# Optimization experiments

Measured on AMD Instinct MI355X. Metric: run time of the kernel, lower is better.

The kernel has to match this reference:

```python
import jax, jax.numpy as jnp
from jax import lax
import numpy as np

D_MODEL = 512
N_HEAD = 8
FACTOR = 5
PRED_LEN = 5
LABEL_LEN = 5
B = 8
SRC_LEN = 2048


def make_pe(max_len, d):
    pos = np.arange(max_len, dtype=np.float32)[:, None]
    div = np.exp(np.arange(0, d, 2, dtype=np.float32) * (-np.log(10000.0) / d))
    pe = np.zeros((max_len, d), dtype=np.float32)
    pe[:, 0::2] = np.sin(pos * div)
    pe[:, 1::2] = np.cos(pos * div)
    return jnp.asarray(pe)


def layer_norm(x, g, b):
    mu = x.mean(-1, keepdims=True)
    var = ((x - mu) ** 2).mean(-1, keepdims=True)
    return (x - mu) / jnp.sqrt(var + 1e-5) * g + b


def prob_attention(q, k, v, key):
    # ProbSparse attention, mask_flag=False (Informer encoder). q,k,v: [B,H,L,E]
    Bq, H, L, E = q.shape
    L_K = k.shape[2]
    U_part = min(FACTOR * int(np.ceil(np.log(L_K))), L_K)
    u = min(FACTOR * int(np.ceil(np.log(L))), L)
    idx = jax.random.randint(key, (L, U_part), 0, L_K)  # sampled key ids per query
    k_samp = k[:, :, idx, :]                             # [B,H,L,U,E]
    qk_samp = jnp.einsum('bhle,bhlue->bhlu', q, k_samp)
    M = qk_samp.max(-1) - qk_samp.sum(-1) / L_K          # sparsity measure [B,H,L]
    _, top_idx = lax.top_k(M, u)                         # [B,H,u]
    q_red = jnp.take_along_axis(q, top_idx[..., None], axis=2)       # [B,H,u,E]
    scores = jnp.einsum('bhue,bhle->bhul', q_red, k) / jnp.sqrt(jnp.asarray(E, q.dtype))
    attn = jax.nn.softmax(scores, axis=-1)
    upd = jnp.einsum('bhul,bhle->bhue', attn, v)
    ctx = jnp.broadcast_to(v.mean(axis=2, keepdims=True), (Bq, H, L, E))
    bi = jnp.arange(Bq)[:, None, None]
    hi = jnp.arange(H)[None, :, None]
    ctx = ctx.at[bi, hi, top_idx].set(upd)               # scatter active queries
    return ctx.transpose(0, 2, 1, 3)                     # [B,L,H,E]


def attn_block(x, wq, bq, wk, bk, wv, bv, wo, bo, key):
    Bx, L, D = x.shape
    E = D // N_HEAD
    q = (x @ wq + bq).reshape(Bx, L, N_HEAD, E).transpose(0, 2, 1, 3)
    k = (x @ wk + bk).reshape(Bx, L, N_HEAD, E).transpose(0, 2, 1, 3)
    v = (x @ wv + bv).reshape(Bx, L, N_HEAD, E).transpose(0, 2, 1, 3)
    ctx = prob_attention(q, k, v, key)
    return ctx.reshape(Bx, L, D) @ wo + bo


def distill(x, w, b, g, beta, rm, rv):
    # circular conv k=3 -> BatchNorm(eval) -> ELU -> maxpool k=3 s=2 p=1
    xc = x.transpose(0, 2, 1)
    xp = jnp.pad(xc, ((0, 0), (0, 0), (1, 1)), mode='wrap')
    y = lax.conv_general_dilated(xp, w, (1,), 'VALID',
                                 dimension_numbers=('NCH', 'OIH', 'NCH')) + b[None, :, None]
    y = (y - rm[None, :, None]) / jnp.sqrt(rv[None, :, None] + 1e-5) * g[None, :, None] + beta[None, :, None]
    y = jax.nn.elu(y)
    y = lax.reduce_window(y, -jnp.inf, lax.max, (1, 1, 3), (1, 1, 2),
                          [(0, 0), (0, 0), (1, 1)])
    return y.transpose(0, 2, 1)


def reference(src, tgt_start, in_w, in_b, conv_w, conv_b,
              wq, bq, wk, bk, wv, bv, wo, bo,
              n1_g, n1_b, ff1_w, ff1_b, ff2_w, ff2_b, n2_g, n2_b,
              dconv_w, dconv_b, bn_g, bn_b, bn_m, bn_v,
              enc_g, enc_b, dec_w, dec_b, head_w, head_b):
    Bx, L, _ = src.shape
    pe = make_pe(5000, D_MODEL)
    x = src @ in_w + in_b + pe[:L][None]
    xc = lax.conv_general_dilated(x.transpose(0, 2, 1), conv_w, (1,), [(1, 1)],
                                  dimension_numbers=('NCH', 'OIH', 'NCH')) + conv_b[None, :, None]
    x = xc.transpose(0, 2, 1)
    base = jax.random.key(42)
    n_layers = wq.shape[0]
    for i in range(n_layers):
        key = jax.random.fold_in(base, i)
        a = attn_block(x, wq[i], bq[i], wk[i], bk[i], wv[i], bv[i], wo[i], bo[i], key)
        x = layer_norm(x + a, n1_g[i], n1_b[i])
        y = jax.nn.gelu(x @ ff1_w[i] + ff1_b[i], approximate=False)
        y = y @ ff2_w[i] + ff2_b[i]
        x = layer_norm(x + y, n2_g[i], n2_b[i])
        if i < n_layers - 1:
            x = distill(x, dconv_w[i], dconv_b[i], bn_g[i], bn_b[i], bn_m[i], bn_v[i])
    memory = layer_norm(x, enc_g, enc_b)
    # decoder side of the source forward (self.decoder is never called there)
    dec_len = LABEL_LEN + PRED_LEN
    y0 = jnp.zeros((Bx, dec_len, 2), src.dtype).at[:, :LABEL_LEN, :].set(tgt_start[:, 0, :][:, None, :])
    pe2 = make_pe(2048, D_MODEL)
    tgt = y0 @ dec_w + dec_b + pe2[:dec_len][None]
    # faithful bug: pos_decoder(tgt, memory) treats batch axis as seq axis
    dec_out = tgt + pe2[:Bx][:, None, :]
    out = dec_out @ head_w + head_b
    pred = out[:, -PRED_LEN:, :]
    return pred, memory


def setup_inputs():
    key = jax.random.key(0)
    ks = iter(jax.random.split(key, 64))

    def w(shape, scale):
        return jax.random.normal(next(ks), shape, jnp.float32) * scale

    L4, L3, D = 4, 3, D_MODEL
    s = 1.0 / np.sqrt(D)
    return dict(
        src=jax.random.normal(next(ks), (B, SRC_LEN, 6), jnp.float32),
        tgt_start=jax.random.normal(next(ks), (B, 1, 2), jnp.float32),
        in_w=w((6, D), 1.0 / np.sqrt(6)), in_b=w((D,), 0.02),
        conv_w=w((D, D, 3), 1.0 / np.sqrt(3 * D)), conv_b=w((D,), 0.02),
        wq=w((L4, D, D), s), bq=w((L4, D), 0.02),
        wk=w((L4, D, D), s), bk=w((L4, D), 0.02),
        wv=w((L4, D, D), s), bv=w((L4, D), 0.02),
        wo=w((L4, D, D), s), bo=w((L4, D), 0.02),
        n1_g=jnp.ones((L4, D)), n1_b=jnp.zeros((L4, D)),
        ff1_w=w((L4, D, D), s), ff1_b=w((L4, D), 0.02),
        ff2_w=w((L4, D, D), s), ff2_b=w((L4, D), 0.02),
        n2_g=jnp.ones((L4, D)), n2_b=jnp.zeros((L4, D)),
        dconv_w=w((L3, D, D, 3), 1.0 / np.sqrt(3 * D)), dconv_b=w((L3, D), 0.02),
        bn_g=jnp.ones((L3, D)), bn_b=jnp.zeros((L3, D)),
        bn_m=jnp.zeros((L3, D)), bn_v=jnp.ones((L3, D)),
        enc_g=jnp.ones((D,)), enc_b=jnp.zeros((D,)),
        dec_w=w((2, D), 1.0 / np.sqrt(2)), dec_b=w((D,), 0.02),
        head_w=w((D, 2), s), head_b=w((2,), 0.02),
    )
```

## Files before the change

kernel.cpp:

```cpp
#include <hip/hip_runtime.h>
#include <hip/hip_bf16.h>
#include <math.h>
#include <stdint.h>

typedef long long ll;

__host__ __device__ inline uint32_t rotl32(uint32_t v, int d) { return (v << d) | (v >> (32 - d)); }

#define TF_R4(a, b, c, d)                              \
  x0 += x1; x1 = rotl32(x1, a); x1 ^= x0;              \
  x0 += x1; x1 = rotl32(x1, b); x1 ^= x0;              \
  x0 += x1; x1 = rotl32(x1, c); x1 ^= x0;              \
  x0 += x1; x1 = rotl32(x1, d); x1 ^= x0;

__host__ __device__ inline void threefry(uint32_t k0, uint32_t k1, uint32_t x0, uint32_t x1,
                                         uint32_t* o0, uint32_t* o1) {
  uint32_t ks2 = k0 ^ k1 ^ 0x1BD11BDAu;
  x0 += k0; x1 += k1;
  TF_R4(13, 15, 26, 6)
  x0 += k1; x1 += ks2 + 1u;
  TF_R4(17, 29, 16, 24)
  x0 += ks2; x1 += k0 + 2u;
  TF_R4(13, 15, 26, 6)
  x0 += k0; x1 += k1 + 3u;
  TF_R4(17, 29, 16, 24)
  x0 += k1; x1 += ks2 + 4u;
  TF_R4(13, 15, 26, 6)
  x0 += ks2; x1 += k0 + 5u;
  *o0 = x0; *o1 = x1;
}

__device__ __forceinline__ float pe_val(int pos, int d) {
  int k2 = (d >> 1) << 1;
  float div = expf((float)k2 * (-9.210340371976184f / 512.0f));
  float arg = (float)pos * div;
  return (d & 1) ? cosf(arg) : sinf(arg);
}


__global__ __launch_bounds__(256) void embed_kernel(const float* __restrict__ src,
                                                    const float* __restrict__ in_w,
                                                    const float* __restrict__ in_b,
                                                    int b0, int nb, float* __restrict__ out) {
  ll i = (ll)blockIdx.x * 256 + threadIdx.x;
  if (i >= (ll)nb * 2048 * 512) return;
  int d = (int)(i & 511);
  ll r = i >> 9;
  int l = (int)(r & 2047);
  int b = b0 + (int)(r >> 11);
  float acc = in_b[d];
#pragma unroll
  for (int j = 0; j < 6; j++)
    acc = fmaf(src[((ll)b * 2048 + l) * 6 + j], in_w[j * 512 + d], acc);
  acc += pe_val(l, d);
  out[i] = acc;
}

__global__ __launch_bounds__(256) void wt_kernel(const float* __restrict__ W,
                                                 float* __restrict__ WT,
                                                 ll srcOff) {
  __shared__ float tile[64][65];
  int o0 = blockIdx.x * 64, c0 = blockIdx.y * 64;
  int t = threadIdx.x;
  int g = t >> 6, l = t & 63;
#pragma unroll 4
  for (int jj = 0; jj < 16; jj++) {
    int r = g * 16 + jj;
    tile[r][l] = W[srcOff + (ll)(o0 + r) * 1536 + (c0 + l)];
  }
  __syncthreads();
#pragma unroll 4
  for (int jj = 0; jj < 16; jj++) {
    int c = g * 16 + jj;
    int gc = c0 + c;
    int tap = gc % 3, k = gc / 3;
    WT[(ll)tap * 262144 + (ll)k * 512 + (o0 + l)] = tile[l][c];
  }
}

__global__ __launch_bounds__(256, 4) void gemm_kernel(
    const float* __restrict__ A, int mBase, int L, int K,
    const float* __restrict__ W, ll wOffBase, int wSK, int wSN, int wTapStride,
    const float* __restrict__ bias, float* __restrict__ C, int N,
    int taps, int shiftMode, int fuse,
    const float* __restrict__ bn_g, const float* __restrict__ bn_b,
    const float* __restrict__ bn_m, const float* __restrict__ bn_v) {
  __shared__ float As[32][68];
  __shared__ float Bs[32][64];
  const int tid = threadIdx.x;
  const int tx = tid & 15, ty = tid >> 4;
  const int m0 = blockIdx.x * 64, n0 = blockIdx.y * 64;
  const int rA = tid >> 2;
  const int kA = (tid & 3) << 3;
  const int kB = tid >> 4, nB0 = (tid & 15) << 2;

  float acc[4][4] = {};

  for (int tp = 0; tp < taps; tp++) {
    int shift = (taps == 3) ? tp - 1 : 0;
    int gRow = mBase + m0 + rA;
    int b = gRow / L, l = gRow - b * L;
    int l2 = l + shift;
    bool valid = true;
    if (shiftMode == 1) { valid = (l2 >= 0 && l2 < L); if (!valid) l2 = 0; }
    else if (shiftMode == 2) { l2 = l2 < 0 ? l2 + L : (l2 >= L ? l2 - L : l2); }
    const float* aRow = A + (ll)(b * L + l2) * K;
    const ll wOff = wOffBase + (taps == 3 ? (ll)tp * wTapStride : 0);

    for (int k0 = 0; k0 < K; k0 += 32) {
      float4 a0 = make_float4(0.f, 0.f, 0.f, 0.f);
      float4 a1 = make_float4(0.f, 0.f, 0.f, 0.f);
      if (valid) {
        a0 = *(const float4*)(aRow + k0 + kA);
        a1 = *(const float4*)(aRow + k0 + kA + 4);
      }
      As[kA + 0][rA] = a0.x; As[kA + 1][rA] = a0.y;
      As[kA + 2][rA] = a0.z; As[kA + 3][rA] = a0.w;
      As[kA + 4][rA] = a1.x; As[kA + 5][rA] = a1.y;
      As[kA + 6][rA] = a1.z; As[kA + 7][rA] = a1.w;
      if (wSN == 1) {
        *(float4*)&Bs[kB][nB0] = *(const float4*)(W + wOff + (ll)(k0 + kB) * wSK + (n0 + nB0));
        *(float4*)&Bs[kB + 16][nB0] = *(const float4*)(W + wOff + (ll)(k0 + kB + 16) * wSK + (n0 + nB0));
      } else {
#pragma unroll
        for (int j = 0; j < 4; j++)
          Bs[kB][nB0 + j] = W[wOff + (ll)(k0 + kB) * wSK + (ll)(n0 + nB0 + j) * wSN];
#pragma unroll
        for (int j = 0; j < 4; j++)
          Bs[kB + 16][nB0 + j] = W[wOff + (ll)(k0 + kB + 16) * wSK + (ll)(n0 + nB0 + j) * wSN];
      }
      __syncthreads();
#pragma unroll
      for (int kk = 0; kk < 32; kk++) {
        float4 w4 = *(const float4*)&Bs[kk][tx << 2];
        float4 a4 = *(const float4*)&As[kk][ty << 2];
        acc[0][0] = fmaf(a4.x, w4.x, acc[0][0]); acc[0][1] = fmaf(a4.x, w4.y, acc[0][1]);
        acc[0][2] = fmaf(a4.x, w4.z, acc[0][2]); acc[0][3] = fmaf(a4.x, w4.w, acc[0][3]);
        acc[1][0] = fmaf(a4.y, w4.x, acc[1][0]); acc[1][1] = fmaf(a4.y, w4.y, acc[1][1]);
        acc[1][2] = fmaf(a4.y, w4.z, acc[1][2]); acc[1][3] = fmaf(a4.y, w4.w, acc[1][3]);
        acc[2][0] = fmaf(a4.z, w4.x, acc[2][0]); acc[2][1] = fmaf(a4.z, w4.y, acc[2][1]);
        acc[2][2] = fmaf(a4.z, w4.z, acc[2][2]); acc[2][3] = fmaf(a4.z, w4.w, acc[2][3]);
        acc[3][0] = fmaf(a4.w, w4.x, acc[3][0]); acc[3][1] = fmaf(a4.w, w4.y, acc[3][1]);
        acc[3][2] = fmaf(a4.w, w4.z, acc[3][2]); acc[3][3] = fmaf(a4.w, w4.w, acc[3][3]);
      }
      __syncthreads();
    }
  }

  float4 bv = make_float4(0.f, 0.f, 0.f, 0.f);
  if (bias) bv = *(const float4*)(bias + n0 + (tx << 2));
  float4 g4, b4, m4, v4;
  if (fuse == 2) {
    g4 = *(const float4*)(bn_g + n0 + (tx << 2));
    b4 = *(const float4*)(bn_b + n0 + (tx << 2));
    m4 = *(const float4*)(bn_m + n0 + (tx << 2));
    v4 = *(const float4*)(bn_v + n0 + (tx << 2));
    v4.x = 1.f / sqrtf(v4.x + 1e-5f); v4.y = 1.f / sqrtf(v4.y + 1e-5f);
    v4.z = 1.f / sqrtf(v4.z + 1e-5f); v4.w = 1.f / sqrtf(v4.w + 1e-5f);
  }
#pragma unroll
  for (int i = 0; i < 4; i++) {
    int m = m0 + (ty << 2) + i;
    float4 v;
    v.x = acc[i][0] + bv.x; v.y = acc[i][1] + bv.y;
    v.z = acc[i][2] + bv.z; v.w = acc[i][3] + bv.w;
    if (fuse == 1) {
      v.x = 0.5f * v.x * (1.f + erff(v.x * 0.70710678118654752f));
      v.y = 0.5f * v.y * (1.f + erff(v.y * 0.70710678118654752f));
      v.z = 0.5f * v.z * (1.f + erff(v.z * 0.70710678118654752f));
      v.w = 0.5f * v.w * (1.f + erff(v.w * 0.70710678118654752f));
    } else if (fuse == 2) {
      v.x = (v.x - m4.x) * v4.x * g4.x + b4.x; v.x = v.x > 0.f ? v.x : expm1f(v.x);
      v.y = (v.y - m4.y) * v4.y * g4.y + b4.y; v.y = v.y > 0.f ? v.y : expm1f(v.y);
      v.z = (v.z - m4.z) * v4.z * g4.z + b4.z; v.z = v.z > 0.f ? v.z : expm1f(v.z);
      v.w = (v.w - m4.w) * v4.w * g4.w + b4.w; v.w = v.w > 0.f ? v.w : expm1f(v.w);
    }
    *(float4*)(C + (ll)m * N + n0 + (tx << 2)) = v;
  }
}

__global__ __launch_bounds__(256, 4) void qkv_kernel(
    const float* __restrict__ X,
    const float* __restrict__ wq, const float* __restrict__ wk, const float* __restrict__ wv,
    ll wOff,
    const float* __restrict__ bq, const float* __restrict__ bk, const float* __restrict__ bv,
    float* __restrict__ QH, float* __restrict__ KH, float* __restrict__ VH) {
  const float* W; const float* bias; float* C;
  if (blockIdx.y == 0) { W = wq; bias = bq; C = QH; }
  else if (blockIdx.y == 1) { W = wk; bias = bk; C = KH; }
  else { W = wv; bias = bv; C = VH; }
  __shared__ float As[32][68];
  __shared__ float Bs[32][64];
  const int tid = threadIdx.x;
  const int tx = tid & 15, ty = tid >> 4;
  const int m0 = blockIdx.x * 64;
  const int rA = tid >> 2;
  const int kA = (tid & 3) << 3;
  const int kB = tid >> 4, nB0 = (tid & 15) << 2;
  const float* aRow = X + (ll)(m0 + rA) * 512;

  float acc[4][4] = {};
  for (int k0 = 0; k0 < 512; k0 += 32) {
    float4 a0 = *(const float4*)(aRow + k0 + kA);
    float4 a1 = *(const float4*)(aRow + k0 + kA + 4);
    As[kA + 0][rA] = a0.x; As[kA + 1][rA] = a0.y;
    As[kA + 2][rA] = a0.z; As[kA + 3][rA] = a0.w;
    As[kA + 4][rA] = a1.x; As[kA + 5][rA] = a1.y;
    As[kA + 6][rA] = a1.z; As[kA + 7][rA] = a1.w;
    *(float4*)&Bs[kB][nB0] = *(const float4*)(W + wOff + (ll)(k0 + kB) * 512 + nB0);
    *(float4*)&Bs[kB + 16][nB0] = *(const float4*)(W + wOff + (ll)(k0 + kB + 16) * 512 + nB0);
    __syncthreads();
#pragma unroll
    for (int kk = 0; kk < 32; kk++) {
      float4 w4 = *(const float4*)&Bs[kk][tx << 2];
      float4 a4 = *(const float4*)&As[kk][ty << 2];
      acc[0][0] = fmaf(a4.x, w4.x, acc[0][0]); acc[0][1] = fmaf(a4.x, w4.y, acc[0][1]);
      acc[0][2] = fmaf(a4.x, w4.z, acc[0][2]); acc[0][3] = fmaf(a4.x, w4.w, acc[0][3]);
      acc[1][0] = fmaf(a4.y, w4.x, acc[1][0]); acc[1][1] = fmaf(a4.y, w4.y, acc[1][1]);
      acc[1][2] = fmaf(a4.y, w4.z, acc[1][2]); acc[1][3] = fmaf(a4.y, w4.w, acc[1][3]);
      acc[2][0] = fmaf(a4.z, w4.x, acc[2][0]); acc[2][1] = fmaf(a4.z, w4.y, acc[2][1]);
      acc[2][2] = fmaf(a4.z, w4.z, acc[2][2]); acc[2][3] = fmaf(a4.z, w4.w, acc[2][3]);
      acc[3][0] = fmaf(a4.w, w4.x, acc[3][0]); acc[3][1] = fmaf(a4.w, w4.y, acc[3][1]);
      acc[3][2] = fmaf(a4.w, w4.z, acc[3][2]); acc[3][3] = fmaf(a4.w, w4.w, acc[3][3]);
    }
    __syncthreads();
  }
  float4 bv4 = *(const float4*)(bias + (tx << 2));
#pragma unroll
  for (int i = 0; i < 4; i++) {
    int m = m0 + (ty << 2) + i;
    float4 v;
    v.x = acc[i][0] + bv4.x; v.y = acc[i][1] + bv4.y;
    v.z = acc[i][2] + bv4.z; v.w = acc[i][3] + bv4.w;
    *(float4*)(C + (ll)m * 64 + (tx << 2)) = v;
  }
}

__global__ void idx_kernel(int* __restrict__ idx, uint32_t k0, uint32_t k1, int n, int mask) {
  int m = blockIdx.x * 256 + threadIdx.x;
  if (m < n) {
    uint32_t o0, o1;
    threefry(k0, k1, 0u, (uint32_t)m, &o0, &o1);
    idx[m] = (int)((o0 ^ o1) & (uint32_t)mask);
  }
}

__global__ __launch_bounds__(256) void m_kernel(const float* __restrict__ Q,
                                                const float* __restrict__ Kk,
                                                const int* __restrict__ idx,
                                                float* __restrict__ M, int L, int U) {
  int wid = (int)(((ll)blockIdx.x * 256 + threadIdx.x) >> 6);
  int lane = threadIdx.x & 63;
  if (wid >= 8 * L) return;
  int b = wid / L, l = wid - b * L;
  float qv = Q[((ll)(b * L + l)) * 64 + lane];
  float mx = -INFINITY, sm = 0.f;
  const int* ip = idx + (ll)l * U;
  int uu = 0;
  for (; uu + 8 <= U; uu += 8) {
    int kr0 = ip[uu] & (L - 1);
    int kr1 = ip[uu + 1] & (L - 1);
    int kr2 = ip[uu + 2] & (L - 1);
    int kr3 = ip[uu + 3] & (L - 1);
    int kr4 = ip[uu + 4] & (L - 1);
    int kr5 = ip[uu + 5] & (L - 1);
    int kr6 = ip[uu + 6] & (L - 1);
    int kr7 = ip[uu + 7] & (L - 1);
    float p0 = qv * Kk[((ll)(b * L + kr0)) * 64 + lane];
    float p1 = qv * Kk[((ll)(b * L + kr1)) * 64 + lane];
    float p2 = qv * Kk[((ll)(b * L + kr2)) * 64 + lane];
    float p3 = qv * Kk[((ll)(b * L + kr3)) * 64 + lane];
    float p4 = qv * Kk[((ll)(b * L + kr4)) * 64 + lane];
    float p5 = qv * Kk[((ll)(b * L + kr5)) * 64 + lane];
    float p6 = qv * Kk[((ll)(b * L + kr6)) * 64 + lane];
    float p7 = qv * Kk[((ll)(b * L + kr7)) * 64 + lane];
#pragma unroll
    for (int d = 32; d > 0; d >>= 1) {
      p0 += __shfl_xor(p0, d);
      p1 += __shfl_xor(p1, d);
      p2 += __shfl_xor(p2, d);
      p3 += __shfl_xor(p3, d);
      p4 += __shfl_xor(p4, d);
      p5 += __shfl_xor(p5, d);
      p6 += __shfl_xor(p6, d);
      p7 += __shfl_xor(p7, d);
    }
    mx = fmaxf(mx, p0); sm += p0;
    mx = fmaxf(mx, p1); sm += p1;
    mx = fmaxf(mx, p2); sm += p2;
    mx = fmaxf(mx, p3); sm += p3;
    mx = fmaxf(mx, p4); sm += p4;
    mx = fmaxf(mx, p5); sm += p5;
    mx = fmaxf(mx, p6); sm += p6;
    mx = fmaxf(mx, p7); sm += p7;
  }
  for (; uu + 4 <= U; uu += 4) {
    int kr0 = ip[uu] & (L - 1);
    int kr1 = ip[uu + 1] & (L - 1);
    int kr2 = ip[uu + 2] & (L - 1);
    int kr3 = ip[uu + 3] & (L - 1);
    float p0 = qv * Kk[((ll)(b * L + kr0)) * 64 + lane];
    float p1 = qv * Kk[((ll)(b * L + kr1)) * 64 + lane];
    float p2 = qv * Kk[((ll)(b * L + kr2)) * 64 + lane];
    float p3 = qv * Kk[((ll)(b * L + kr3)) * 64 + lane];
#pragma unroll
    for (int d = 32; d > 0; d >>= 1) {
      p0 += __shfl_xor(p0, d);
      p1 += __shfl_xor(p1, d);
      p2 += __shfl_xor(p2, d);
      p3 += __shfl_xor(p3, d);
    }
    mx = fmaxf(mx, p0); sm += p0;
    mx = fmaxf(mx, p1); sm += p1;
    mx = fmaxf(mx, p2); sm += p2;
    mx = fmaxf(mx, p3); sm += p3;
  }
  for (; uu + 2 <= U; uu += 2) {
    int kr0 = ip[uu] & (L - 1);
    int kr1 = ip[uu + 1] & (L - 1);
    float p0 = qv * Kk[((ll)(b * L + kr0)) * 64 + lane];
    float p1 = qv * Kk[((ll)(b * L + kr1)) * 64 + lane];
#pragma unroll
    for (int d = 32; d > 0; d >>= 1) {
      p0 += __shfl_xor(p0, d);
      p1 += __shfl_xor(p1, d);
    }
    mx = fmaxf(mx, p0); sm += p0;
    mx = fmaxf(mx, p1); sm += p1;
  }
  if (uu < U) {
    int kr = ip[uu] & (L - 1);
    float p = qv * Kk[((ll)(b * L + kr)) * 64 + lane];
#pragma unroll
    for (int d = 32; d > 0; d >>= 1) p += __shfl_xor(p, d);
    mx = fmaxf(mx, p);
    sm += p;
  }
  if (lane == 0) M[(ll)b * L + l] = mx - sm / (float)L;
}

template <int NRT>
__global__ __launch_bounds__(256) void tgv_kernel(const float* __restrict__ M,
                                                  const float* __restrict__ Q,
                                                  const float* __restrict__ V,
                                                  int* __restrict__ topi,
                                                  float* __restrict__ QR,
                                                  float* __restrict__ vm, int L, int u) {
  __shared__ unsigned long long wbest[2][4];
  __shared__ int rows[40];
  __shared__ float s4[4][64];
  int b = blockIdx.x, t = threadIdx.x;
  int lane = t & 63, w = t >> 6;
  ll base = (ll)b * L;
  float v8[NRT];
#pragma unroll
  for (int i = 0; i < NRT; i++) v8[i] = M[base + t + (i << 8)];
  for (int j = 0; j < u; j++) {
    float bv = v8[0]; int bi = t;
#pragma unroll
    for (int i = 1; i < NRT; i++) {
      if (v8[i] > bv) { bv = v8[i]; bi = t + (i << 8); }
    }
    uint32_t mu = __float_as_uint(bv);
    mu = (mu & 0x80000000u) ? ~mu : (mu | 0x80000000u);
    unsigned long long key = ((unsigned long long)mu << 32) | (uint32_t)(~bi);
#pragma unroll
    for (int d = 32; d > 0; d >>= 1) {
      unsigned long long o = __shfl_xor(key, d);
      key = o > key ? o : key;
    }
    if (lane == 0) wbest[j & 1][w] = key;
    __syncthreads();
    unsigned long long k0 = wbest[j & 1][0], k1 = wbest[j & 1][1];
    unsigned long long k2 = wbest[j & 1][2], k3 = wbest[j & 1][3];
    unsigned long long kb = k0 > k1 ? k0 : k1;
    unsigned long long kc = k2 > k3 ? k2 : k3;
    if (kc > kb) kb = kc;
    int wi = (int)(~(uint32_t)kb);
#pragma unroll
    for (int i = 0; i < NRT; i++)
      if (wi == t + (i << 8)) v8[i] = -INFINITY;
    if (t == 0) { topi[(ll)b * u + j] = wi; rows[j] = wi; }
  }
  __syncthreads();
  for (int idx = t; idx < u * 64; idx += 256) {
    int j = idx >> 6, e = idx & 63;
    int row = rows[j];
    QR[((ll)b * u + j) * 64 + e] = Q[((ll)(b * L + row)) * 64 + e];
  }
  int e = t & 63, p2 = t >> 6;
  float acc = 0.f;
  for (int l = p2; l < L; l += 4) acc += V[((ll)(b * L + l)) * 64 + e];
  s4[p2][e] = acc;
  __syncthreads();
  if (t < 64)
    vm[(ll)b * 64 + t] = (s4[0][t] + s4[1][t] + s4[2][t] + s4[3][t]) / (float)L;
}


__global__ __launch_bounds__(256) void attna_kernel(const float* __restrict__ QR,
                                                    const float* __restrict__ Kk,
                                                    float* __restrict__ SCb,
                                                    float* __restrict__ MX,
                                                    int L, int u) {
  int g = blockIdx.x, c = blockIdx.y;
  int b = g / u;
  __shared__ float qs[64];
  __shared__ float wmax[4];
  int t = threadIdx.x;
  if (t < 64) qs[t] = QR[(ll)g * 64 + t];
  __syncthreads();
  int l = (c << 8) + t;
  const float4* kr = (const float4*)(Kk + ((ll)(b * L + l)) * 64);
  float d = 0.f;
#pragma unroll
  for (int e = 0; e < 16; e++) {
    float4 k4 = kr[e];
    float4 q4 = *(const float4*)&qs[e << 2];
    d = fmaf(q4.x, k4.x, d);
    d = fmaf(q4.y, k4.y, d);
    d = fmaf(q4.z, k4.z, d);
    d = fmaf(q4.w, k4.w, d);
  }
  d *= 0.125f;
  SCb[(ll)g * L + l] = d;
  float m = d;
#pragma unroll
  for (int s = 32; s > 0; s >>= 1) m = fmaxf(m, __shfl_xor(m, s));
  if ((t & 63) == 0) wmax[t >> 6] = m;
  __syncthreads();
  if (t == 0)
    MX[g * 8 + c] = fmaxf(fmaxf(wmax[0], wmax[1]), fmaxf(wmax[2], wmax[3]));
}

__global__ __launch_bounds__(256) void attnb_kernel(const float* __restrict__ SCb,
                                                    const float* __restrict__ MX,
                                                    const float* __restrict__ V,
                                                    float* __restrict__ PUPD,
                                                    float* __restrict__ PSUM,
                                                    int L, int u, int C) {
  int g = blockIdx.x, c = blockIdx.y;
  int b = g / u;
  __shared__ float evs[256];
  __shared__ float red[256];
  __shared__ float upds[4][64];
  int t = threadIdx.x;
  float mx = MX[g * 8];
  for (int j = 1; j < C; j++) mx = fmaxf(mx, MX[g * 8 + j]);
  int l = (c << 8) + t;
  float ev = expf(SCb[(ll)g * L + l] - mx);
  evs[t] = ev;
  red[t] = ev;
  __syncthreads();
  for (int s = 128; s > 0; s >>= 1) { if (t < s) red[t] += red[t + s]; __syncthreads(); }
  int e = t & 63, p2 = t >> 6;
  const float* vb = V + ((ll)(b * L + (c << 8))) * 64;
  float partial = 0.f;
#pragma unroll 4
  for (int i = 0; i < 64; i++) {
    int lidx = p2 + (i << 2);
    partial = fmaf(evs[lidx], vb[(ll)lidx * 64 + e], partial);
  }
  upds[p2][e] = partial;
  __syncthreads();
  if (t < 64) {
    PUPD[((ll)(g * 8 + c)) * 64 + t] = upds[0][t] + upds[1][t] + upds[2][t] + upds[3][t];
    if (t == 0) PSUM[g * 8 + c] = red[0];
  }
}

__global__ __launch_bounds__(64) void attnc_kernel(const float* __restrict__ PUPD,
                                                   const float* __restrict__ PSUM,
                                                   float* __restrict__ upd, int C) {
  int g = blockIdx.x, t = threadIdx.x;
  float den = 0.f, val = 0.f;
  for (int c = 0; c < C; c++) {
    den += PSUM[g * 8 + c];
    val += PUPD[((ll)(g * 8 + c)) * 64 + t];
  }
  upd[(ll)g * 64 + t] = val * (1.f / den);
}

__global__ __launch_bounds__(512) void baserow_kernel(const float* __restrict__ VM,
                                                      const float* __restrict__ Wo, ll wOff,
                                                      const float* __restrict__ bo,
                                                      float* __restrict__ BR) {
  int b = blockIdx.x, t = threadIdx.x;
  float acc = bo[t];
  for (int h = 0; h < 8; h++)
#pragma unroll 4
    for (int e = 0; e < 64; e++)
      acc = fmaf(VM[(ll)(h * 8 + b) * 64 + e], Wo[wOff + (ll)(h * 64 + e) * 512 + t], acc);
  BR[(ll)b * 512 + t] = acc;
}

__global__ __launch_bounds__(512) void corr_kernel(const float* __restrict__ UPD,
                                                   const float* __restrict__ VM,
                                                   const int* __restrict__ topi,
                                                   const float* __restrict__ Wo, ll wOff,
                                                   float* __restrict__ X, int L, int u) {
  int g = blockIdx.x;
  int h = g / (8 * u);
  int r = g - h * 8 * u;
  int b = r / u;
  int row = topi[g] & (L - 1);
  int t = threadIdx.x;
  float c = 0.f;
#pragma unroll 4
  for (int e = 0; e < 64; e++) {
    float dv = UPD[(ll)g * 64 + e] - VM[(ll)(h * 8 + b) * 64 + e];
    c = fmaf(dv, Wo[wOff + (ll)(h * 64 + e) * 512 + t], c);
  }
  atomicAdd(&X[((ll)b * L + row) * 512 + t], c);
}

__global__ __launch_bounds__(256) void ln_kernel(const float* __restrict__ x,
                                                 const float* __restrict__ res,
                                                 const float* __restrict__ br, int L,
                                                 const float* __restrict__ g,
                                                 const float* __restrict__ be,
                                                 float* __restrict__ out) {
  ll base = (ll)blockIdx.x * 512;
  int t = threadIdx.x;
  float v0 = x[base + t], v1 = x[base + 256 + t];
  if (res) { v0 += res[base + t]; v1 += res[base + 256 + t]; }
  if (br) {
    int b = blockIdx.x / L;
    v0 += br[(ll)b * 512 + t];
    v1 += br[(ll)b * 512 + 256 + t];
  }
  __shared__ float red[256];
  red[t] = v0 + v1;
  __syncthreads();
  for (int s = 128; s > 0; s >>= 1) { if (t < s) red[t] += red[t + s]; __syncthreads(); }
  float mu = red[0] * (1.f / 512.f);
  __syncthreads();
  float d0 = v0 - mu, d1 = v1 - mu;
  red[t] = d0 * d0 + d1 * d1;
  __syncthreads();
  for (int s = 128; s > 0; s >>= 1) { if (t < s) red[t] += red[t + s]; __syncthreads(); }
  float rstd = 1.f / sqrtf(red[0] * (1.f / 512.f) + 1e-5f);
  out[base + t] = d0 * rstd * g[t] + be[t];
  out[base + 256 + t] = d1 * rstd * g[t + 256] + be[t + 256];
}

__global__ __launch_bounds__(256) void maxpool_kernel(const float* __restrict__ y,
                                                      float* __restrict__ outp,
                                                      int L, int L2, int nb) {
  ll n = (ll)nb * L2 * 512;
  ll i = (ll)blockIdx.x * 256 + threadIdx.x;
  if (i >= n) return;
  int per = L2 * 512;
  int bb = (int)(i / per);
  int rem = (int)(i - (ll)bb * per);
  int c = rem & 511;
  int l2 = rem >> 9;
  int l0 = 2 * l2 - 1;
  float m = -INFINITY;
#pragma unroll
  for (int w = 0; w < 3; w++) {
    int l = l0 + w;
    if (l >= 0 && l < L) m = fmaxf(m, y[((ll)bb * L + l) * 512 + c]);
  }
  outp[i] = m;
}

__global__ __launch_bounds__(64) void pred_kernel(const float* __restrict__ dec_b,
                                                  const float* __restrict__ head_w,
                                                  const float* __restrict__ head_b,
                                                  float* __restrict__ out) {
  int b = blockIdx.x / 5, tt = blockIdx.x % 5, t = 5 + tt;
  int lane = threadIdx.x;
  float a0 = 0.f, a1 = 0.f;
  for (int d = lane; d < 512; d += 64) {
    float td = dec_b[d] + pe_val(t, d) + pe_val(b, d);
    a0 = fmaf(td, head_w[2 * d], a0);
    a1 = fmaf(td, head_w[2 * d + 1], a1);
  }
#pragma unroll
  for (int s = 32; s > 0; s >>= 1) { a0 += __shfl_xor(a0, s); a1 += __shfl_xor(a1, s); }
  if (lane == 0) {
    out[(ll)b * 10 + tt * 2 + 0] = a0 + head_b[0];
    out[(ll)b * 10 + tt * 2 + 1] = a1 + head_b[1];
  }
}

extern "C" void kernel_launch(void* const* d_in, const int* in_sizes, int n_in,
                              void* d_out, int out_size, void* d_ws, size_t ws_size,
                              hipStream_t stream) {
  if (n_in < 34) return;
  if (in_sizes[0] != 8 * 2048 * 6) return;
  if (in_sizes[4] != 512 * 512 * 3) return;
  if (in_sizes[6] != 4 * 512 * 512) return;
  if (in_sizes[22] != 3 * 512 * 512 * 3) return;
  if (in_sizes[33] != 2) return;
  if (ws_size < 55700000) return;

  const ll BIG = (ll)8 * 2048 * 512;
  const ll HSZ = (ll)8 * 2048 * 64;
  const ll CSZ = (ll)2048 * 512;

  const float* src    = (const float*)d_in[0];
  const float* in_w   = (const float*)d_in[2];
  const float* in_b   = (const float*)d_in[3];
  const float* conv_w = (const float*)d_in[4];
  const float* conv_b = (const float*)d_in[5];
  const float* wq = (const float*)d_in[6];
  const float* bq = (const float*)d_in[7];
  const float* wk = (const float*)d_in[8];
  const float* bk = (const float*)d_in[9];
  const float* wv = (const float*)d_in[10];
  const float* bv = (const float*)d_in[11];
  const float* wo = (const float*)d_in[12];
  const float* bo = (const float*)d_in[13];
  const float* n1_g = (const float*)d_in[14];
  const float* n1_b = (const float*)d_in[15];
  const float* ff1_w = (const float*)d_in[16];
  const float* ff1_b = (const float*)d_in[17];
  const float* ff2_w = (const float*)d_in[18];
  const float* ff2_b = (const float*)d_in[19];
  const float* n2_g = (const float*)d_in[20];
  const float* n2_b = (const float*)d_in[21];
  const float* dconv_w = (const float*)d_in[22];
  const float* dconv_b = (const float*)d_in[23];
  const float* bn_g = (const float*)d_in[24];
  const float* bn_b = (const float*)d_in[25];
  const float* bn_m = (const float*)d_in[26];
  const float* bn_v = (const float*)d_in[27];
  const float* enc_g = (const float*)d_in[28];
  const float* enc_b = (const float*)d_in[29];
  const float* dec_bv = (const float*)d_in[31];
  const float* head_w = (const float*)d_in[32];
  const float* head_b = (const float*)d_in[33];
  float* out = (float*)d_out;

  char* p = (char*)d_ws;
  float* X  = (float*)p; p += BIG * 4;
  float* QH = (float*)p; p += HSZ * 4;
  float* KH = (float*)p; p += HSZ * 4;
  float* VH = (float*)p; p += HSZ * 4;
  float* SC1 = (float*)p; p += CSZ * 4;
  float* SC2 = (float*)p; p += CSZ * 4;
  float* UPD = (float*)p; p += (ll)8 * 8 * 40 * 64 * 4;
  float* VM  = (float*)p; p += (ll)8 * 8 * 64 * 4;
  float* BR  = (float*)p; p += (ll)8 * 512 * 4;
  float* Mh  = (float*)p; p += (ll)8 * 2048 * 4;
  float* QR  = (float*)p; p += (ll)8 * 40 * 64 * 4;
  int* IDX   = (int*)p; p += (ll)2048 * 40 * 4;
  int* TOPIA = (int*)p;

  float* P0 = QH;
  float* P1 = QH + (ll)4096 * 512;
  float* MXf   = SC2;
  float* PSUMf = SC2 + 4096;
  float* PUPDf = SC2 + 8192;
  float* WT = SC2;

  uint32_t keys[4][2];
  for (int i = 0; i < 4; i++) {
    uint32_t K0, K1, g0, g1;
    threefry(0u, 42u, 0u, (uint32_t)i, &K0, &K1);
    threefry(K0, K1, 0u, 1u, &g0, &g1);
    keys[i][0] = g0;
    keys[i][1] = g1;
  }

  wt_kernel<<<dim3(8, 24), 256, 0, stream>>>(conv_w, WT, 0);
  for (int bp = 0; bp < 4; bp++) {
    embed_kernel<<<(int)((2 * CSZ + 255) / 256), 256, 0, stream>>>(src, in_w, in_b, bp * 2, 2, P0);
    gemm_kernel<<<dim3(64, 8), 256, 0, stream>>>(
        P0, 0, 2048, 512, WT, 0, 512, 1, 262144, conv_b, X + (ll)bp * 2 * CSZ, 512,
        3, 1, 0, nullptr, nullptr, nullptr, nullptr);
  }

  const int Ls[4] = {2048, 1024, 512, 256};
  const int Us[4] = {40, 35, 35, 30};

  for (int i = 0; i < 4; i++) {
    int L = Ls[i], U = Us[i];
    int Mrows = 8 * L;
    int LU = L * U;
    int C = L >> 8;
    ll wOff = (ll)i * 262144;

    idx_kernel<<<(LU + 255) / 256, 256, 0, stream>>>(IDX, keys[i][0], keys[i][1], LU, L - 1);

    for (int h = 0; h < 8; h++) {
      qkv_kernel<<<dim3(Mrows / 64, 3), 256, 0, stream>>>(
          X, wq, wk, wv, wOff + h * 64,
          bq + i * 512 + h * 64, bk + i * 512 + h * 64, bv + i * 512 + h * 64, QH, KH, VH);
      m_kernel<<<(8 * L * 64) / 256, 256, 0, stream>>>(QH, KH, IDX, Mh, L, U);
      if (L == 2048)
        tgv_kernel<8><<<8, 256, 0, stream>>>(Mh, QH, VH, TOPIA + (ll)h * 8 * U, QR,
                                             VM + (ll)h * 8 * 64, L, U);
      else if (L == 1024)
        tgv_kernel<4><<<8, 256, 0, stream>>>(Mh, QH, VH, TOPIA + (ll)h * 8 * U, QR,
                                             VM + (ll)h * 8 * 64, L, U);
      else if (L == 512)
        tgv_kernel<2><<<8, 256, 0, stream>>>(Mh, QH, VH, TOPIA + (ll)h * 8 * U, QR,
                                             VM + (ll)h * 8 * 64, L, U);
      else
        tgv_kernel<1><<<8, 256, 0, stream>>>(Mh, QH, VH, TOPIA + (ll)h * 8 * U, QR,
                                             VM + (ll)h * 8 * 64, L, U);
      attna_kernel<<<dim3(8 * U, C), 256, 0, stream>>>(QR, KH, SC1, MXf, L, U);
      attnb_kernel<<<dim3(8 * U, C), 256, 0, stream>>>(SC1, MXf, VH, PUPDf, PSUMf, L, U, C);
      attnc_kernel<<<8 * U, 64, 0, stream>>>(PUPDf, PSUMf, UPD + (ll)h * 8 * U * 64, C);
    }

    baserow_kernel<<<8, 512, 0, stream>>>(VM, wo, wOff, bo + i * 512, BR);
    corr_kernel<<<64 * U, 512, 0, stream>>>(UPD, VM, TOPIA, wo, wOff, X, L, U);
    ln_kernel<<<Mrows, 256, 0, stream>>>(X, nullptr, BR, L, n1_g + i * 512, n1_b + i * 512, X);

    int CR = Mrows < 4096 ? Mrows : 4096;
    for (int r0 = 0; r0 < Mrows; r0 += CR) {
      gemm_kernel<<<dim3(CR / 64, 8), 256, 0, stream>>>(
          X + (ll)r0 * 512, 0, CR, 512, ff1_w, wOff, 512, 1, 0, ff1_b + i * 512, P0, 512,
          1, 0, 1, nullptr, nullptr, nullptr, nullptr);
      gemm_kernel<<<dim3(CR / 64, 8), 256, 0, stream>>>(
          P0, 0, CR, 512, ff2_w, wOff, 512, 1, 0, ff2_b + i * 512, P1, 512,
          1, 0, 0, nullptr, nullptr, nullptr, nullptr);
      ln_kernel<<<CR, 256, 0, stream>>>(X + (ll)r0 * 512, P1, nullptr, L, n2_g + i * 512,
                                        n2_b + i * 512, X + (ll)r0 * 512);
    }

    if (i < 3) {
      wt_kernel<<<dim3(8, 24), 256, 0, stream>>>(dconv_w, WT, (ll)i * 786432);
      int L2 = L / 2;
      int nbc = 4096 / L; if (nbc > 8) nbc = 8;
      for (int bp = 0; bp < 8 / nbc; bp++) {
        gemm_kernel<<<dim3((nbc * L) / 64, 8), 256, 0, stream>>>(
            X, bp * nbc * L, L, 512, WT, 0, 512, 1, 262144, dconv_b + i * 512,
            P0, 512, 3, 2, 2, bn_g + i * 512, bn_b + i * 512, bn_m + i * 512, bn_v + i * 512);
        maxpool_kernel<<<(int)(((ll)nbc * L2 * 512 + 255) / 256), 256, 0, stream>>>(
            P0, X + (ll)bp * nbc * L2 * 512, L, L2, nbc);
      }
    }
  }

  ln_kernel<<<8 * 256, 256, 0, stream>>>(X, nullptr, nullptr, 256, enc_g, enc_b, out + 80);
  pred_kernel<<<40, 64, 0, stream>>>(dec_bv, head_w, head_b, out);
}
```

Before: 7.270 ms.

## Reuse K rows in registers across all selected queries in attna kernel

```diff
diff --git a/kernel.cpp b/kernel.cpp
--- a/kernel.cpp
+++ b/kernel.cpp
@@ -397,40 +397,48 @@
     vm[(ll)b * 64 + t] = (s4[0][t] + s4[1][t] + s4[2][t] + s4[3][t]) / (float)L;
 }
 
+#define QKDOT(i) { float4 qq = q4[i]; \
+  d = fmaf(qq.x, krr##i.x, d); d = fmaf(qq.y, krr##i.y, d); \
+  d = fmaf(qq.z, krr##i.z, d); d = fmaf(qq.w, krr##i.w, d); }
 
 __global__ __launch_bounds__(256) void attna_kernel(const float* __restrict__ QR,
                                                     const float* __restrict__ Kk,
                                                     float* __restrict__ SCb,
                                                     float* __restrict__ MX,
                                                     int L, int u) {
-  int g = blockIdx.x, c = blockIdx.y;
-  int b = g / u;
-  __shared__ float qs[64];
-  __shared__ float wmax[4];
+  int b = blockIdx.x, c = blockIdx.y;
   int t = threadIdx.x;
-  if (t < 64) qs[t] = QR[(ll)g * 64 + t];
+  int lane = t & 63, w = t >> 6;
+  __shared__ float qs[40 * 64];
+  __shared__ float wmax[2][4];
+  for (int idx = t; idx < u * 64; idx += 256)
+    qs[idx] = QR[(ll)(b * u) * 64 + idx];
   __syncthreads();
   int l = (c << 8) + t;
   const float4* kr = (const float4*)(Kk + ((ll)(b * L + l)) * 64);
-  float d = 0.f;
-#pragma unroll
-  for (int e = 0; e < 16; e++) {
-    float4 k4 = kr[e];
-    float4 q4 = *(const float4*)&qs[e << 2];
-    d = fmaf(q4.x, k4.x, d);
-    d = fmaf(q4.y, k4.y, d);
-    d = fmaf(q4.z, k4.z, d);
-    d = fmaf(q4.w, k4.w, d);
-  }
-  d *= 0.125f;
-  SCb[(ll)g * L + l] = d;
-  float m = d;
-#pragma unroll
-  for (int s = 32; s > 0; s >>= 1) m = fmaxf(m, __shfl_xor(m, s));
-  if ((t & 63) == 0) wmax[t >> 6] = m;
-  __syncthreads();
-  if (t == 0)
-    MX[g * 8 + c] = fmaxf(fmaxf(wmax[0], wmax[1]), fmaxf(wmax[2], wmax[3]));
+  float4 krr0 = kr[0],  krr1 = kr[1],  krr2 = kr[2],  krr3 = kr[3];
+  float4 krr4 = kr[4],  krr5 = kr[5],  krr6 = kr[6],  krr7 = kr[7];
+  float4 krr8 = kr[8],  krr9 = kr[9],  krr10 = kr[10], krr11 = kr[11];
+  float4 krr12 = kr[12], krr13 = kr[13], krr14 = kr[14], krr15 = kr[15];
+  for (int j = 0; j < u; j++) {
+    const float4* q4 = (const float4*)&qs[j << 6];
+    float d = 0.f;
+    QKDOT(0)  QKDOT(1)  QKDOT(2)  QKDOT(3)
+    QKDOT(4)  QKDOT(5)  QKDOT(6)  QKDOT(7)
+    QKDOT(8)  QKDOT(9)  QKDOT(10) QKDOT(11)
+    QKDOT(12) QKDOT(13) QKDOT(14) QKDOT(15)
+    d *= 0.125f;
+    SCb[(ll)(b * u + j) * L + l] = d;
+    float m = d;
+#pragma unroll
+    for (int s = 32; s > 0; s >>= 1) m = fmaxf(m, __shfl_xor(m, s));
+    if (lane == 0) wmax[j & 1][w] = m;
+    __syncthreads();
+    if (t == 0)
+      MX[(b * u + j) * 8 + c] =
+          fmaxf(fmaxf(wmax[j & 1][0], wmax[j & 1][1]),
+                fmaxf(wmax[j & 1][2], wmax[j & 1][3]));
+  }
 }
 
 __global__ __launch_bounds__(256) void attnb_kernel(const float* __restrict__ SCb,
@@ -702,7 +710,7 @@
       else
         tgv_kernel<1><<<8, 256, 0, stream>>>(Mh, QH, VH, TOPIA + (ll)h * 8 * U, QR,
                                              VM + (ll)h * 8 * 64, L, U);
-      attna_kernel<<<dim3(8 * U, C), 256, 0, stream>>>(QR, KH, SC1, MXf, L, U);
+      attna_kernel<<<dim3(8, C), 256, 0, stream>>>(QR, KH, SC1, MXf, L, U);
       attnb_kernel<<<dim3(8 * U, C), 256, 0, stream>>>(SC1, MXf, VH, PUPDf, PSUMf, L, U, C);
       attnc_kernel<<<8 * U, 64, 0, stream>>>(PUPDf, PSUMf, UPD + (ll)h * 8 * U * 64, C);
     }
```

Result: slower. 7.799 ms (+7.3%).
